# Performance work log

Measured on AMD Instinct MI355X. Metric: run time of the kernel, lower is better.

## Reference

```python
import jax, jax.numpy as jnp
import numpy as np

EPS = 1e-20
BETA = 0.25


def setup_inputs() -> dict:
    key = jax.random.key(0)
    k1, k2, k3 = jax.random.split(key, 3)
    B, N, D = 8192, 8192, 512
    x = jax.random.normal(k1, (B, D), dtype=jnp.float32)
    codebook = jax.random.normal(k2, (N, D), dtype=jnp.float32)
    u = jax.random.uniform(k3, (B, N), dtype=jnp.float32)
    return {"x": x, "codebook": codebook, "u": u}


def reference(x, codebook, u):
    # gumbel noise from uniform samples (matches sample_gumble)
    g = -jnp.log(-jnp.log(u + EPS) + EPS)  # [B, N]
    dist = (jnp.sum(x * x, axis=1, keepdims=True)
            - 2.0 * (x @ codebook.T)
            + jnp.sum(codebook * codebook, axis=1)[None, :])
    # topk(k=1) over -dist == argmin over dist
    ind = jnp.argmin(dist, axis=1)  # [B]
    # gumbel_softmax with temperature=1.0 on logits=-dist
    weights = jax.nn.softmax(-dist + g, axis=-1)  # [B, N]
    quantized = weights @ codebook  # [B, D]
    sg = jax.lax.stop_gradient
    loss = (BETA * jnp.sum((x - sg(quantized)) ** 2, axis=-1)
            + jnp.sum((sg(x) - quantized) ** 2, axis=-1))  # [B]
    return quantized, ind, loss
```

## Files before the change

kernel.cpp:

```cpp
#include <hip/hip_runtime.h>
#include <math.h>

constexpr int B = 8192, N = 8192, D = 512;
constexpr float EPSF = 1e-20f;
constexpr float SKIP   = 20.0f;
constexpr float DELTAF = 1.0f;
constexpr float DELTA  = 0.05f;
constexpr int CAP  = 96;
constexpr int DCAP = 48;

typedef short bf16x8 __attribute__((ext_vector_type(8)));
typedef float f32x4 __attribute__((ext_vector_type(4)));

__device__ inline unsigned short f2bf(float f) {
    unsigned x = __float_as_uint(f);
    unsigned r = x + 0x7FFFu + ((x >> 16) & 1u);
    return (unsigned short)(r >> 16);
}
__device__ inline float bf2f(unsigned short h) {
    return __uint_as_float(((unsigned)h) << 16);
}
__device__ inline unsigned fmap(float f) {
    unsigned b = __float_as_uint(f);
    return b ^ ((unsigned)((int)b >> 31) | 0x80000000u);
}
__device__ inline float funmap(unsigned u) {
    unsigned b = u ^ ((~(unsigned)((int)u >> 31)) | 0x80000000u);
    return __uint_as_float(b);
}
__device__ inline void gload16(const void* g, void* l) {
    __builtin_amdgcn_global_load_lds(
        (const __attribute__((address_space(1))) void*)g,
        (__attribute__((address_space(3))) void*)l, 16, 0, 0);
}


__global__ __launch_bounds__(256) void vq_prep(const float* __restrict__ x,
        const float* __restrict__ cb, unsigned short* __restrict__ ch,
        float* __restrict__ cnorm, float* __restrict__ xnorm,
        int* __restrict__ counts, int* __restrict__ dcounts) {
    int w = threadIdx.x >> 6, lane = threadIdx.x & 63;
    int gid = blockIdx.x * 256 + threadIdx.x;
    if (gid < 2 * B) { counts[gid] = 0; dcounts[gid] = 0; }
    int v = blockIdx.x * 4 + w;
    if (v < N) {
        const float4* s4 = reinterpret_cast<const float4*>(cb + (size_t)v * D) + lane * 2;
        float4 a = s4[0], c = s4[1];
        float vals[8] = {a.x, a.y, a.z, a.w, c.x, c.y, c.z, c.w};
        float ns = 0.f;
        unsigned short hb[8];
        #pragma unroll
        for (int e = 0; e < 8; ++e) {
            float vv = vals[e];
            ns += vv * vv;
            hb[e] = f2bf(vv);
        }
        #pragma unroll
        for (int off = 1; off < 64; off <<= 1) ns += __shfl_xor(ns, off);
        if (lane == 0) cnorm[v] = ns;
        *reinterpret_cast<bf16x8*>(ch + (size_t)v * D + lane * 8) = *reinterpret_cast<bf16x8*>(hb);
    } else {
        int b = v - N;
        const float4* s4 = reinterpret_cast<const float4*>(x + (size_t)b * D) + lane * 2;
        float4 a = s4[0], c = s4[1];
        float ns = a.x*a.x + a.y*a.y + a.z*a.z + a.w*a.w
                 + c.x*c.x + c.y*c.y + c.z*c.z + c.w*c.w;
        #pragma unroll
        for (int off = 1; off < 64; off <<= 1) ns += __shfl_xor(ns, off);
        if (lane == 0) xnorm[b] = ns;
    }
}

constexpr int OFF_B0 = 0;
constexpr int OFF_B1 = 65536;
constexpr int OFF_RM = 131072;
constexpr int OFF_R1 = 131328;
constexpr int OFF_CT = 131584;
constexpr int OFF_DC = 131840;
constexpr int OFF_P1 = 132096;
constexpr int OFF_P2 = 132608;
constexpr int OFF_PI = 133120;
constexpr int SMEM_BYTES = 133632;

__global__ __launch_bounds__(512, 1) void vq_mfma(
        const float* __restrict__ x, const unsigned short* __restrict__ ch,
        const float* __restrict__ cnorm, const float* __restrict__ xnorm,
        const float* __restrict__ u,
        int2* __restrict__ lists, int* __restrict__ counts,
        int* __restrict__ dlists, int* __restrict__ dcounts,
        float* __restrict__ m1h, float* __restrict__ m2h, int* __restrict__ i1h) {

    __shared__ __align__(16) unsigned char smem[SMEM_BYTES];

    const int tid = threadIdx.x, w = tid >> 6, lane = tid & 63;
    const int wm = w >> 1, wn = w & 1, l15 = lane & 15, g = lane >> 4;
    const int rg = blockIdx.x >> 1, half = blockIdx.x & 1;
    const int rbase = rg * 64, nb0 = half * 4096;

    bf16x8 ah[16];
    {
        const float* xp = x + (size_t)(rbase + wm * 16 + l15) * D + g * 8;
        #pragma unroll
        for (int ks = 0; ks < 16; ++ks) {
            const float4* p = reinterpret_cast<const float4*>(xp + ks * 32);
            float4 v0 = p[0], v1 = p[1];
            float vv[8] = {v0.x, v0.y, v0.z, v0.w, v1.x, v1.y, v1.z, v1.w};
            unsigned short hh[8];
            #pragma unroll
            for (int e = 0; e < 8; ++e) hh[e] = f2bf(vv[e]);
            ah[ks] = *reinterpret_cast<bf16x8*>(hh);
        }
    }
    float xn_r[4];
    #pragma unroll
    for (int r = 0; r < 4; ++r) xn_r[r] = xnorm[rbase + wm * 16 + g * 4 + r];

    if (tid < 64) {
        *(unsigned*)(smem + OFF_RM + tid * 4) = fmap(-INFINITY);
        *(unsigned*)(smem + OFF_R1 + tid * 4) = fmap(INFINITY);
        *(int*)(smem + OFF_CT + tid * 4) = 0;
        *(int*)(smem + OFF_DC + tid * 4) = 0;
    }

    float d1[4], d2[4], lmax[4]; int i1[4];
    #pragma unroll
    for (int r = 0; r < 4; ++r) {
        d1[r] = INFINITY; d2[r] = INFINITY; lmax[r] = -INFINITY; i1[r] = 0;
    }

    auto stage = [&](unsigned char* bbase, int nbn) {
        #pragma unroll
        for (int j = 0; j < 8; ++j) {
            const int row = w * 8 + j;
            const int c = (lane ^ j) * 8;
            gload16(ch + (size_t)(nbn + row) * D + c, bbase + row * 1024);
        }
    };

    stage(smem + OFF_B0, nb0);
    __syncthreads();

    const int colA = wn * 32 + l15;
    const int xr = colA & 7;

    #pragma unroll 1
    for (int t = 0; t < 64; ++t) {
        const int nb = nb0 + t * 64;
        if (t < 63) stage(smem + ((t & 1) ? OFF_B0 : OFF_B1), nb + 64);

        float ur[2][4];
        #pragma unroll
        for (int f = 0; f < 2; ++f)
            #pragma unroll
            for (int r = 0; r < 4; ++r)
                ur[f][r] = u[(size_t)(rbase + wm * 16 + g * 4 + r) * N + nb + wn * 32 + f * 16 + l15];
        float cn0 = cnorm[nb + wn * 32 + l15];
        float cn1 = cnorm[nb + wn * 32 + 16 + l15];

        const unsigned char* baseH = smem + ((t & 1) ? OFF_B1 : OFF_B0) + colA * 1024;
        f32x4 a0e = {0.f,0.f,0.f,0.f}, a0o = {0.f,0.f,0.f,0.f};
        f32x4 a1e = {0.f,0.f,0.f,0.f}, a1o = {0.f,0.f,0.f,0.f};
        #pragma unroll
        for (int ks = 0; ks < 16; ++ks) {
            const int pos = (((ks * 4 + g) ^ xr) << 4);
            bf16x8 b0 = *reinterpret_cast<const bf16x8*>(baseH + pos);
            bf16x8 b1 = *reinterpret_cast<const bf16x8*>(baseH + 16 * 1024 + pos);
            if (ks & 1) {
                a0o = __builtin_amdgcn_mfma_f32_16x16x32_bf16(ah[ks], b0, a0o, 0, 0, 0);
                a1o = __builtin_amdgcn_mfma_f32_16x16x32_bf16(ah[ks], b1, a1o, 0, 0, 0);
            } else {
                a0e = __builtin_amdgcn_mfma_f32_16x16x32_bf16(ah[ks], b0, a0e, 0, 0, 0);
                a1e = __builtin_amdgcn_mfma_f32_16x16x32_bf16(ah[ks], b1, a1e, 0, 0, 0);
            }
        }

        float dsv[2][4], lgv[2][4];
        #pragma unroll
        for (int f = 0; f < 2; ++f) {
            #pragma unroll
            for (int r = 0; r < 4; ++r) {
                float S = f ? (a1e[r] + a1o[r]) : (a0e[r] + a0o[r]);
                float ds = xn_r[r] - 2.f * S + (f ? cn1 : cn0);
                float gn = -__logf(-__logf(ur[f][r] + EPSF) + EPSF);
                dsv[f][r] = ds; lgv[f][r] = gn - ds;
            }
        }
        #pragma unroll
        for (int f = 0; f < 2; ++f)
            #pragma unroll
            for (int r = 0; r < 4; ++r) {
                float ds = dsv[f][r];
                int cidx = nb + wn * 32 + f * 16 + l15;
                if (ds < d1[r]) { d2[r] = d1[r]; d1[r] = ds; i1[r] = cidx; }
                else if (ds < d2[r]) d2[r] = ds;
                lmax[r] = fmaxf(lmax[r], lgv[f][r]);
            }
        if (t == 0) {
            #pragma unroll
            for (int r = 0; r < 4; ++r) {
                float mx = lmax[r], mn = d1[r];
                #pragma unroll
                for (int off = 1; off < 16; off <<= 1) {
                    mx = fmaxf(mx, __shfl_xor(mx, off));
                    mn = fminf(mn, __shfl_xor(mn, off));
                }
                if (l15 == 0) {
                    int rl = wm * 16 + g * 4 + r;
                    atomicMax((unsigned*)(smem + OFF_RM + rl * 4), fmap(mx));
                    atomicMin((unsigned*)(smem + OFF_R1 + rl * 4), fmap(mn));
                }
            }
            __syncthreads();
        }
        float rmF[4], r1F[4];
        #pragma unroll
        for (int r = 0; r < 4; ++r) {
            int rl = wm * 16 + g * 4 + r;
            rmF[r] = funmap(*(const unsigned*)(smem + OFF_RM + rl * 4));
            r1F[r] = funmap(*(const unsigned*)(smem + OFF_R1 + rl * 4));
        }
        #pragma unroll
        for (int f = 0; f < 2; ++f) {
            #pragma unroll
            for (int r = 0; r < 4; ++r) {
                const int rl = wm * 16 + g * 4 + r;
                const int grow = rbase + rl;
                float ds = dsv[f][r], lg = lgv[f][r];
                int cidx = nb + wn * 32 + f * 16 + l15;
                if (ds < fminf(r1F[r], d1[r]) + DELTAF) {
                    int slot = atomicAdd((int*)(smem + OFF_DC + rl * 4), 1);
                    if (slot < DCAP) dlists[(size_t)(half * B + grow) * DCAP + slot] = cidx;
                }
                if (ds < r1F[r]) atomicMin((unsigned*)(smem + OFF_R1 + rl * 4), fmap(ds));
                if (lg > fmaxf(rmF[r], lmax[r]) - SKIP) {
                    int slot = atomicAdd((int*)(smem + OFF_CT + rl * 4), 1);
                    if (slot < CAP)
                        lists[(size_t)(half * B + grow) * CAP + slot] =
                            make_int2(__float_as_int(lg), cidx);
                }
                if (lg > rmF[r]) atomicMax((unsigned*)(smem + OFF_RM + rl * 4), fmap(lg));
            }
        }
        __syncthreads();
    }

    #pragma unroll
    for (int r = 0; r < 4; ++r) {
        float D1 = d1[r], D2v = d2[r]; int I1 = i1[r];
        #pragma unroll
        for (int off = 1; off < 16; off <<= 1) {
            float o1 = __shfl_xor(D1, off), o2 = __shfl_xor(D2v, off);
            int oi = __shfl_xor(I1, off);
            if (o1 < D1 || (o1 == D1 && oi < I1)) { D2v = fminf(D1, o2); D1 = o1; I1 = oi; }
            else D2v = fminf(o1, D2v);
        }
        if (l15 == 0) {
            int rl = wm * 16 + g * 4 + r;
            *(float*)(smem + OFF_P1 + (wn * 64 + rl) * 4) = D1;
            *(float*)(smem + OFF_P2 + (wn * 64 + rl) * 4) = D2v;
            *(int*)(smem + OFF_PI + (wn * 64 + rl) * 4) = I1;
        }
    }
    __syncthreads();
    if (tid < 64) {
        float a1 = *(float*)(smem + OFF_P1 + tid * 4), a2 = *(float*)(smem + OFF_P2 + tid * 4);
        int ai = *(int*)(smem + OFF_PI + tid * 4);
        float b1 = *(float*)(smem + OFF_P1 + (64 + tid) * 4), b2 = *(float*)(smem + OFF_P2 + (64 + tid) * 4);
        int bi = *(int*)(smem + OFF_PI + (64 + tid) * 4);
        float m1, m2; int mi;
        if (b1 < a1 || (b1 == a1 && bi < ai)) { m1 = b1; mi = bi; m2 = fminf(a1, b2); }
        else                                  { m1 = a1; mi = ai; m2 = fminf(b1, a2); }
        int hrow = half * B + rbase + tid;
        m1h[hrow] = m1; m2h[hrow] = m2; i1h[hrow] = mi;
        counts[hrow] = *(int*)(smem + OFF_CT + tid * 4);
        dcounts[hrow] = *(int*)(smem + OFF_DC + tid * 4);
    }
}

__global__ __launch_bounds__(256) void vq_finalize(
        const float* __restrict__ cb, const float* __restrict__ x,
        const int2* __restrict__ lists, const int* __restrict__ counts,
        float* __restrict__ m1h, float* __restrict__ m2h, int* __restrict__ i1h,
        float* __restrict__ out_q, float* __restrict__ out_loss) {
    __shared__ int2 ebuf[4][2 * CAP];
    int w = threadIdx.x >> 6, lane = threadIdx.x & 63;
    int row = blockIdx.x * 4 + w;
    int n0 = counts[row];      if (n0 > CAP) n0 = CAP;
    int n1 = counts[B + row];  if (n1 > CAP) n1 = CAP;
    int n = n0 + n1;
    for (int e = lane; e < n0; e += 64) ebuf[w][e] = lists[(size_t)row * CAP + e];
    for (int e = lane; e < n1; e += 64) ebuf[w][n0 + e] = lists[(size_t)(B + row) * CAP + e];
    __syncthreads();
    float m = -INFINITY;
    for (int e = lane; e < n; e += 64) m = fmaxf(m, __int_as_float(ebuf[w][e].x));
    #pragma unroll
    for (int off = 1; off < 64; off <<= 1) m = fmaxf(m, __shfl_xor(m, off));
    float denom = 0.f;
    for (int e = lane; e < n; e += 64) denom += __expf(__int_as_float(ebuf[w][e].x) - m);
    #pragma unroll
    for (int off = 1; off < 64; off <<= 1) denom += __shfl_xor(denom, off);
    float q[8] = {0.f, 0.f, 0.f, 0.f, 0.f, 0.f, 0.f, 0.f};
    for (int e = 0; e < n; ++e) {
        int2 ent = ebuf[w][e];
        float wgt = __expf(__int_as_float(ent.x) - m);
        if (wgt < 1e-9f) continue;
        const float4* c4 = reinterpret_cast<const float4*>(cb + (size_t)ent.y * D + lane * 8);
        float4 c0 = c4[0], c1 = c4[1];
        q[0] += wgt * c0.x; q[1] += wgt * c0.y; q[2] += wgt * c0.z; q[3] += wgt * c0.w;
        q[4] += wgt * c1.x; q[5] += wgt * c1.y; q[6] += wgt * c1.z; q[7] += wgt * c1.w;
    }
    float inv = 1.f / denom;
    const float4* x4 = reinterpret_cast<const float4*>(x + (size_t)row * D + lane * 8);
    float4 xa = x4[0], xb = x4[1];
    float xs[8] = {xa.x, xa.y, xa.z, xa.w, xb.x, xb.y, xb.z, xb.w};
    float ls = 0.f;
    #pragma unroll
    for (int k = 0; k < 8; ++k) {
        q[k] *= inv;
        float dlt = xs[k] - q[k];
        ls += dlt * dlt;
    }
    float4 q0 = {q[0], q[1], q[2], q[3]}, q1 = {q[4], q[5], q[6], q[7]};
    float4* o = reinterpret_cast<float4*>(out_q + (size_t)row * D + lane * 8);
    o[0] = q0; o[1] = q1;
    #pragma unroll
    for (int off = 1; off < 64; off <<= 1) ls += __shfl_xor(ls, off);
    if (lane == 0) {
        out_loss[row] = 1.25f * ls;
        float a1 = m1h[row], a2 = m2h[row]; int ai = i1h[row];
        float b1 = m1h[B + row], b2 = m2h[B + row]; int bi = i1h[B + row];
        float mm1, mm2; int mi;
        if (b1 < a1 || (b1 == a1 && bi < ai)) { mm1 = b1; mi = bi; mm2 = fminf(a1, b2); }
        else                                  { mm1 = a1; mi = ai; mm2 = fminf(b1, a2); }
        m1h[row] = mm1; m2h[row] = mm2; i1h[row] = mi;
    }
}

__global__ __launch_bounds__(256) void vq_row_full(
        const float* __restrict__ x, const float* __restrict__ cb,
        const float* __restrict__ cnorm, const float* __restrict__ u,
        const int* __restrict__ counts,
        float* __restrict__ out_q, float* __restrict__ out_loss) {
    int row = blockIdx.x;
    if (counts[row] <= CAP && counts[B + row] <= CAP) return;
    int tid = threadIdx.x, wv_ = tid >> 6, lane = tid & 63;
    __shared__ float xs[D];
    __shared__ float red[4];
    __shared__ float wts[256]; __shared__ int ids[256]; __shared__ int nc;
    for (int i = tid; i < D; i += 256) xs[i] = x[(size_t)row * D + i];
    if (tid == 0) nc = 0;
    __syncthreads();
    float xn = 0.f;
    for (int i = tid; i < D; i += 256) xn += xs[i] * xs[i];
    #pragma unroll
    for (int off = 1; off < 64; off <<= 1) xn += __shfl_xor(xn, off);
    if (lane == 0) red[wv_] = xn;
    __syncthreads();
    xn = red[0] + red[1] + red[2] + red[3];
    __syncthreads();
    float m = -INFINITY;
    for (int n = tid; n < N; n += 256) {
        float dot = 0.f;
        const float* c = cb + (size_t)n * D;
        for (int d = 0; d < D; ++d) dot = fmaf(xs[d], c[d], dot);
        float lg = -__logf(-__logf(u[(size_t)row * N + n] + EPSF) + EPSF)
                 - (xn - 2.f * dot + cnorm[n]);
        m = fmaxf(m, lg);
    }
    #pragma unroll
    for (int off = 1; off < 64; off <<= 1) m = fmaxf(m, __shfl_xor(m, off));
    if (lane == 0) red[wv_] = m;
    __syncthreads();
    m = fmaxf(fmaxf(red[0], red[1]), fmaxf(red[2], red[3]));
    __syncthreads();
    float denom = 0.f;
    for (int n = tid; n < N; n += 256) {
        float dot = 0.f;
        const float* c = cb + (size_t)n * D;
        for (int d = 0; d < D; ++d) dot = fmaf(xs[d], c[d], dot);
        float lg = -__logf(-__logf(u[(size_t)row * N + n] + EPSF) + EPSF)
                 - (xn - 2.f * dot + cnorm[n]);
        float wv2 = __expf(lg - m);
        denom += wv2;
        if (wv2 > 1e-8f) {
            int s = atomicAdd(&nc, 1);
            if (s < 256) { wts[s] = wv2; ids[s] = n; }
        }
    }
    #pragma unroll
    for (int off = 1; off < 64; off <<= 1) denom += __shfl_xor(denom, off);
    if (lane == 0) red[wv_] = denom;
    __syncthreads();
    denom = red[0] + red[1] + red[2] + red[3];
    int ncl = nc < 256 ? nc : 256;
    float q0 = 0.f, q1 = 0.f;
    for (int e = 0; e < ncl; ++e) {
        const float* c = cb + (size_t)ids[e] * D;
        q0 += wts[e] * c[tid * 2];
        q1 += wts[e] * c[tid * 2 + 1];
    }
    q0 /= denom; q1 /= denom;
    out_q[(size_t)row * D + tid * 2] = q0;
    out_q[(size_t)row * D + tid * 2 + 1] = q1;
    float dl0 = xs[tid * 2] - q0, dl1 = xs[tid * 2 + 1] - q1;
    float ls = dl0 * dl0 + dl1 * dl1;
    #pragma unroll
    for (int off = 1; off < 64; off <<= 1) ls += __shfl_xor(ls, off);
    __syncthreads();
    if (lane == 0) red[wv_] = ls;
    __syncthreads();
    if (tid == 0) out_loss[row] = 1.25f * (red[0] + red[1] + red[2] + red[3]);
}

__global__ __launch_bounds__(256) void argmin_fix2(
        const float* __restrict__ x, const float* __restrict__ cb,
        const float* __restrict__ m1h, const float* __restrict__ m2h,
        const int* __restrict__ i1h,
        const int* __restrict__ dcounts, const int* __restrict__ dlists,
        float* __restrict__ out_ind) {
    int w = threadIdx.x >> 6, lane = threadIdx.x & 63;
    int row = blockIdx.x * 4 + w;
    if (m2h[row] - m1h[row] >= DELTAF) {
        if (lane == 0) out_ind[row] = (float)i1h[row];
        return;
    }
    const float4* x4 = reinterpret_cast<const float4*>(x + (size_t)row * D) + lane * 2;
    float4 xa = x4[0], xb = x4[1];
    double xd[8] = {(double)xa.x, (double)xa.y, (double)xa.z, (double)xa.w,
                    (double)xb.x, (double)xb.y, (double)xb.z, (double)xb.w};
    double bestv = 1e300; int besti = 0x7fffffff;

    auto evalCode = [&](int n) {
        const float4* c4 = reinterpret_cast<const float4*>(cb + (size_t)n * D) + lane * 2;
        float4 ca = c4[0], cbv = c4[1];
        double cd[8] = {(double)ca.x, (double)ca.y, (double)ca.z, (double)ca.w,
                        (double)cbv.x, (double)cbv.y, (double)cbv.z, (double)cbv.w};
        double s = 0.0;
        #pragma unroll
        for (int k = 0; k < 8; ++k) {
            double dlt = xd[k] - cd[k];
            s = fma(dlt, dlt, s);
        }
        #pragma unroll
        for (int off = 1; off < 64; off <<= 1) s += __shfl_xor(s, off);
        if (s < bestv || (s == bestv && n < besti)) { bestv = s; besti = n; }
    };

    int n0 = dcounts[row], n1 = dcounts[B + row];
    if (n0 <= DCAP && n1 <= DCAP) {
        evalCode(i1h[row]);
        for (int e = 0; e < n0; ++e) evalCode(dlists[(size_t)row * DCAP + e]);
        for (int e = 0; e < n1; ++e) evalCode(dlists[(size_t)(B + row) * DCAP + e]);
    } else {
        for (int n = 0; n < N; ++n) evalCode(n);
    }
    if (lane == 0) out_ind[row] = (float)besti;
}

constexpr int ROWS = 16;
constexpr int NT   = 256;
constexpr int DT   = 16;

__global__ __launch_bounds__(256) void prep_norms(const float* __restrict__ x,
                                                  const float* __restrict__ cb,
                                                  float* __restrict__ cnorm,
                                                  float* __restrict__ xnorm) {
    int wave = threadIdx.x >> 6, lane = threadIdx.x & 63;
    int v = blockIdx.x * 4 + wave;
    const float* src;
    float* dst;
    if (v < N) { src = cb + (size_t)v * D; dst = cnorm + v; }
    else       { int b = v - N; if (b >= B) return; src = x + (size_t)b * D; dst = xnorm + b; }
    const float4* s4 = reinterpret_cast<const float4*>(src) + lane * 2;
    float4 a = s4[0], c = s4[1];
    float s = a.x*a.x + a.y*a.y + a.z*a.z + a.w*a.w
            + c.x*c.x + c.y*c.y + c.z*c.z + c.w*c.w;
    #pragma unroll
    for (int off = 1; off < 64; off <<= 1) s += __shfl_xor(s, off);
    if (lane == 0) *dst = s;
}

__global__ __launch_bounds__(256) void vq_main(const float* __restrict__ x,
        const float* __restrict__ cb, const float* __restrict__ u,
        const float* __restrict__ cnorm, const float* __restrict__ xnorm,
        float* __restrict__ out_q, float* __restrict__ out_loss,
        float* __restrict__ m1w, float* __restrict__ m2w, int* __restrict__ i1w) {

    __shared__ float xs[ROWS][D];
    __shared__ float ct[DT][NT];

    const int tid  = threadIdx.x;
    const int wave = tid >> 6, lane = tid & 63;
    const int rbase = blockIdx.x * ROWS;
    const int wrow  = rbase + wave * 4;

    for (int i = tid; i < ROWS * (D / 4); i += 256)
        reinterpret_cast<float4*>(xs)[i] =
            reinterpret_cast<const float4*>(x + (size_t)rbase * D)[i];
    __syncthreads();

    float xn[4];
    #pragma unroll
    for (int r = 0; r < 4; ++r) xn[r] = xnorm[wrow + r];

    float m[4], denom[4], acc[4][8];
    float am1[4], am2[4]; int ai1[4];
    #pragma unroll
    for (int r = 0; r < 4; ++r) {
        m[r] = -INFINITY; denom[r] = 0.f;
        am1[r] = INFINITY; am2[r] = INFINITY; ai1[r] = 0;
        #pragma unroll
        for (int k = 0; k < 8; ++k) acc[r][k] = 0.f;
    }

    for (int nb = 0; nb < N; nb += NT) {
        float S[4][4];
        #pragma unroll
        for (int r = 0; r < 4; ++r)
            #pragma unroll
            for (int j = 0; j < 4; ++j) S[r][j] = 0.f;

        for (int db = 0; db < D; db += DT) {
            __syncthreads();
            {
                const float4* src = reinterpret_cast<const float4*>(
                        cb + (size_t)(nb + tid) * D + db);
                float4 a0 = src[0], a1 = src[1], a2 = src[2], a3 = src[3];
                ct[ 0][tid]=a0.x; ct[ 1][tid]=a0.y; ct[ 2][tid]=a0.z; ct[ 3][tid]=a0.w;
                ct[ 4][tid]=a1.x; ct[ 5][tid]=a1.y; ct[ 6][tid]=a1.z; ct[ 7][tid]=a1.w;
                ct[ 8][tid]=a2.x; ct[ 9][tid]=a2.y; ct[10][tid]=a2.z; ct[11][tid]=a2.w;
                ct[12][tid]=a3.x; ct[13][tid]=a3.y; ct[14][tid]=a3.z; ct[15][tid]=a3.w;
            }
            __syncthreads();
            #pragma unroll
            for (int dq = 0; dq < DT / 4; ++dq) {
                float creg[4][4];
                #pragma unroll
                for (int k = 0; k < 4; ++k) {
                    float4 cv = *reinterpret_cast<const float4*>(&ct[dq*4 + k][4*lane]);
                    creg[k][0]=cv.x; creg[k][1]=cv.y; creg[k][2]=cv.z; creg[k][3]=cv.w;
                }
                #pragma unroll
                for (int r = 0; r < 4; ++r) {
                    float4 xv = *reinterpret_cast<const float4*>(&xs[wave*4 + r][db + dq*4]);
                    float xr[4] = {xv.x, xv.y, xv.z, xv.w};
                    #pragma unroll
                    for (int k = 0; k < 4; ++k)
                        #pragma unroll
                        for (int j = 0; j < 4; ++j)
                            S[r][j] = fmaf(xr[k], creg[k][j], S[r][j]);
                }
            }
        }

        float4 cn4 = *reinterpret_cast<const float4*>(&cnorm[nb + 4*lane]);
        float cn[4] = {cn4.x, cn4.y, cn4.z, cn4.w};

        float logit[4][4], dist[4][4];
        #pragma unroll
        for (int r = 0; r < 4; ++r) {
            float4 u4 = *reinterpret_cast<const float4*>(
                    &u[(size_t)(wrow + r) * N + nb + 4*lane]);
            float uu[4] = {u4.x, u4.y, u4.z, u4.w};
            #pragma unroll
            for (int j = 0; j < 4; ++j) {
                float ds = xn[r] - 2.f * S[r][j] + cn[j];
                float gg  = -logf(-logf(uu[j] + EPSF) + EPSF);
                dist[r][j]  = ds;
                logit[r][j] = gg - ds;
            }
        }

        #pragma unroll
        for (int r = 0; r < 4; ++r) {
            float l1 = INFINITY, l2 = INFINITY; int li = 0;
            #pragma unroll
            for (int j = 0; j < 4; ++j) {
                float dv = dist[r][j]; int idx = nb + 4*lane + j;
                if (dv < l1)      { l2 = l1; l1 = dv; li = idx; }
                else if (dv < l2) { l2 = dv; }
            }
            #pragma unroll
            for (int off = 1; off < 64; off <<= 1) {
                float o1 = __shfl_xor(l1, off), o2 = __shfl_xor(l2, off);
                int   oi = __shfl_xor(li, off);
                if (o1 < l1 || (o1 == l1 && oi < li)) { l2 = fminf(l1, o2); l1 = o1; li = oi; }
                else                                  { l2 = fminf(o1, l2); }
            }
            if (l1 < am1[r] || (l1 == am1[r] && li < ai1[r])) {
                am2[r] = fminf(am1[r], l2); am1[r] = l1; ai1[r] = li;
            } else {
                am2[r] = fminf(am2[r], l1);
            }

            float lm = fmaxf(fmaxf(logit[r][0], logit[r][1]),
                             fmaxf(logit[r][2], logit[r][3]));
            #pragma unroll
            for (int off = 1; off < 64; off <<= 1) lm = fmaxf(lm, __shfl_xor(lm, off));
            if (lm > m[r]) {
                float s = expf(m[r] - lm);
                denom[r] *= s;
                #pragma unroll
                for (int k = 0; k < 8; ++k) acc[r][k] *= s;
                m[r] = lm;
            }

            float wv[4];
            #pragma unroll
            for (int j = 0; j < 4; ++j) {
                float e = logit[r][j] - m[r];
                bool act = e > -SKIP;
                wv[j] = act ? expf(e) : 0.f;
                denom[r] += wv[j];
            }
            #pragma unroll
            for (int j = 0; j < 4; ++j) {
                unsigned long long mk = __ballot(wv[j] > 0.f);
                while (mk) {
                    int L = __ffsll((unsigned long long)mk) - 1;
                    mk &= mk - 1;
                    float wb = __shfl(wv[j], L);
                    int nstar = nb + 4*L + j;
                    const float4* crow = reinterpret_cast<const float4*>(
                            cb + (size_t)nstar * D + 8*lane);
                    float4 c0 = crow[0], c1 = crow[1];
                    acc[r][0] = fmaf(wb, c0.x, acc[r][0]);
                    acc[r][1] = fmaf(wb, c0.y, acc[r][1]);
                    acc[r][2] = fmaf(wb, c0.z, acc[r][2]);
                    acc[r][3] = fmaf(wb, c0.w, acc[r][3]);
                    acc[r][4] = fmaf(wb, c1.x, acc[r][4]);
                    acc[r][5] = fmaf(wb, c1.y, acc[r][5]);
                    acc[r][6] = fmaf(wb, c1.z, acc[r][6]);
                    acc[r][7] = fmaf(wb, c1.w, acc[r][7]);
                }
            }
        }
    }

    #pragma unroll
    for (int r = 0; r < 4; ++r) {
        float dn = denom[r];
        #pragma unroll
        for (int off = 1; off < 64; off <<= 1) dn += __shfl_xor(dn, off);
        float inv = 1.f / dn;
        int row = wrow + r;
        float q[8]; float ls = 0.f;
        #pragma unroll
        for (int k = 0; k < 8; ++k) {
            q[k] = acc[r][k] * inv;
            float dlt = xs[wave*4 + r][8*lane + k] - q[k];
            ls += dlt * dlt;
        }
        float4 q0 = {q[0], q[1], q[2], q[3]}, q1 = {q[4], q[5], q[6], q[7]};
        float4* o = reinterpret_cast<float4*>(out_q + (size_t)row * D + 8*lane);
        o[0] = q0; o[1] = q1;
        #pragma unroll
        for (int off = 1; off < 64; off <<= 1) ls += __shfl_xor(ls, off);
        if (lane == 0) {
            out_loss[row] = 1.25f * ls;
            m1w[row] = am1[r]; m2w[row] = am2[r]; i1w[row] = ai1[r];
        }
    }
}

__global__ __launch_bounds__(256) void argmin_fix(const float* __restrict__ x,
        const float* __restrict__ cb, const float* __restrict__ m1w,
        const float* __restrict__ m2w, const int* __restrict__ i1w,
        float* __restrict__ out_ind) {
    int b = blockIdx.x, tid = threadIdx.x;
    if (m2w[b] - m1w[b] >= DELTA) {
        if (tid == 0) out_ind[b] = (float)i1w[b];
        return;
    }
    __shared__ double xsd[D];
    for (int i = tid; i < D; i += 256) xsd[i] = (double)x[(size_t)b * D + i];
    __syncthreads();
    double xn = 0.0;
    for (int d = 0; d < D; ++d) xn += xsd[d] * xsd[d];

    double bestv = 1e300; int besti = N;
    for (int n = tid; n < N; n += 256) {
        const float* c = cb + (size_t)n * D;
        double d0 = 0.0, d1v = 0.0, c0 = 0.0, c1v = 0.0;
        for (int d = 0; d < D; d += 2) {
            double ca = (double)c[d], cbv = (double)c[d + 1];
            d0 += xsd[d] * ca;  c0 += ca * ca;
            d1v += xsd[d + 1] * cbv; c1v += cbv * cbv;
        }
        double dv = xn - 2.0 * (d0 + d1v) + (c0 + c1v);
        if (dv < bestv || (dv == bestv && n < besti)) { bestv = dv; besti = n; }
    }
    __shared__ double rv[256]; __shared__ int ri[256];
    rv[tid] = bestv; ri[tid] = besti;
    __syncthreads();
    for (int s = 128; s > 0; s >>= 1) {
        if (tid < s) {
            if (rv[tid+s] < rv[tid] || (rv[tid+s] == rv[tid] && ri[tid+s] < ri[tid])) {
                rv[tid] = rv[tid+s]; ri[tid] = ri[tid+s];
            }
        }
        __syncthreads();
    }
    if (tid == 0) out_ind[b] = (float)ri[0];
}

extern "C" void kernel_launch(void* const* d_in, const int* in_sizes, int n_in,
                              void* d_out, int out_size, void* d_ws, size_t ws_size,
                              hipStream_t stream) {
    const float* x  = (const float*)d_in[0];
    const float* cb = (const float*)d_in[1];
    const float* u  = (const float*)d_in[2];
    float* out      = (float*)d_out;
    float* out_q    = out;
    float* out_ind  = out + (size_t)B * D;
    float* out_loss = out_ind + B;

    const size_t O_CH = 0;
    const size_t O_CN = O_CH + (size_t)N * D * 2;
    const size_t O_XN = O_CN + (size_t)N * 4;
    const size_t O_M1 = O_XN + (size_t)B * 4;
    const size_t O_M2 = O_M1 + (size_t)2 * B * 4;
    const size_t O_I1 = O_M2 + (size_t)2 * B * 4;
    const size_t O_CT = O_I1 + (size_t)2 * B * 4;
    const size_t O_DC = O_CT + (size_t)2 * B * 4;
    const size_t O_LS = O_DC + (size_t)2 * B * 4;
    const size_t O_DL = O_LS + (size_t)2 * B * CAP * 8;
    const size_t NEED = O_DL + (size_t)2 * B * DCAP * 4;

    if (ws_size >= NEED) {
        char* w8 = (char*)d_ws;
        unsigned short* ch = (unsigned short*)(w8 + O_CH);
        float* cnorm = (float*)(w8 + O_CN);
        float* xnorm = (float*)(w8 + O_XN);
        float* m1h   = (float*)(w8 + O_M1);
        float* m2h   = (float*)(w8 + O_M2);
        int*   i1h   = (int*)(w8 + O_I1);
        int*   counts= (int*)(w8 + O_CT);
        int*   dcounts=(int*)(w8 + O_DC);
        int2*  lists = (int2*)(w8 + O_LS);
        int*   dlists= (int*)(w8 + O_DL);

        hipLaunchKernelGGL(vq_prep, dim3((N + B) / 4), dim3(256), 0, stream,
                           x, cb, ch, cnorm, xnorm, counts, dcounts);
        hipLaunchKernelGGL(vq_mfma, dim3(256), dim3(512), 0, stream,
                           x, ch, cnorm, xnorm, u, lists, counts,
                           dlists, dcounts, m1h, m2h, i1h);
        hipLaunchKernelGGL(vq_finalize, dim3(B / 4), dim3(256), 0, stream,
                           cb, x, lists, counts, m1h, m2h, i1h, out_q, out_loss);
        hipLaunchKernelGGL(vq_row_full, dim3(B), dim3(256), 0, stream,
                           x, cb, cnorm, u, counts, out_q, out_loss);
        hipLaunchKernelGGL(argmin_fix2, dim3(B / 4), dim3(256), 0, stream,
                           x, cb, m1h, m2h, i1h, dcounts, dlists, out_ind);
    } else {
        float* ws    = (float*)d_ws;
        float* cnorm = ws;
        float* xnorm = ws + N;
        float* m1w   = xnorm + B;
        float* m2w   = m1w + B;
        int*   i1w   = (int*)(m2w + B);

        hipLaunchKernelGGL(prep_norms, dim3((N + B) / 4), dim3(256), 0, stream,
                           x, cb, cnorm, xnorm);
        hipLaunchKernelGGL(vq_main, dim3(B / ROWS), dim3(256), 0, stream,
                           x, cb, u, cnorm, xnorm, out_q, out_loss, m1w, m2w, i1w);
        hipLaunchKernelGGL(argmin_fix, dim3(B), dim3(256), 0, stream,
                           x, cb, m1w, m2w, i1w, out_ind);
    }
}
```

Baseline: 302.9 us.

## Prefetch uniform noise one tile ahead and skip Gumbel logs for hopeless candidates

```diff
diff --git a/kernel.cpp b/kernel.cpp
--- a/kernel.cpp
+++ b/kernel.cpp
@@ -4,6 +4,7 @@
 constexpr int B = 8192, N = 8192, D = 512;
 constexpr float EPSF = 1e-20f;
 constexpr float SKIP   = 20.0f;
+constexpr float GMAX   = 17.0f;
 constexpr float DELTAF = 1.0f;
 constexpr float DELTA  = 0.05f;
 constexpr int CAP  = 96;
@@ -138,6 +139,15 @@
     };
 
     stage(smem + OFF_B0, nb0);
+
+    const float* ubase = u + (size_t)(rbase + wm * 16 + g * 4) * N + wn * 32 + l15;
+    float ur[2][4];
+    #pragma unroll
+    for (int f = 0; f < 2; ++f)
+        #pragma unroll
+        for (int r = 0; r < 4; ++r)
+            ur[f][r] = ubase[(size_t)r * N + f * 16 + nb0];
+
     __syncthreads();
 
     const int colA = wn * 32 + l15;
@@ -148,12 +158,14 @@
         const int nb = nb0 + t * 64;
         if (t < 63) stage(smem + ((t & 1) ? OFF_B0 : OFF_B1), nb + 64);
 
-        float ur[2][4];
-        #pragma unroll
-        for (int f = 0; f < 2; ++f)
-            #pragma unroll
-            for (int r = 0; r < 4; ++r)
-                ur[f][r] = u[(size_t)(rbase + wm * 16 + g * 4 + r) * N + nb + wn * 32 + f * 16 + l15];
+        float urN[2][4];
+        if (t < 63) {
+            #pragma unroll
+            for (int f = 0; f < 2; ++f)
+                #pragma unroll
+                for (int r = 0; r < 4; ++r)
+                    urN[f][r] = ubase[(size_t)r * N + f * 16 + nb + 64];
+        }
         float cn0 = cnorm[nb + wn * 32 + l15];
         float cn1 = cnorm[nb + wn * 32 + 16 + l15];
 
@@ -174,28 +186,29 @@
             }
         }
 
-        float dsv[2][4], lgv[2][4];
-        #pragma unroll
-        for (int f = 0; f < 2; ++f) {
+        float dsv[2][4];
+        #pragma unroll
+        for (int f = 0; f < 2; ++f)
             #pragma unroll
             for (int r = 0; r < 4; ++r) {
                 float S = f ? (a1e[r] + a1o[r]) : (a0e[r] + a0o[r]);
-                float ds = xn_r[r] - 2.f * S + (f ? cn1 : cn0);
-                float gn = -__logf(-__logf(ur[f][r] + EPSF) + EPSF);
-                dsv[f][r] = ds; lgv[f][r] = gn - ds;
-            }
-        }
-        #pragma unroll
-        for (int f = 0; f < 2; ++f)
-            #pragma unroll
-            for (int r = 0; r < 4; ++r) {
-                float ds = dsv[f][r];
-                int cidx = nb + wn * 32 + f * 16 + l15;
-                if (ds < d1[r]) { d2[r] = d1[r]; d1[r] = ds; i1[r] = cidx; }
-                else if (ds < d2[r]) d2[r] = ds;
-                lmax[r] = fmaxf(lmax[r], lgv[f][r]);
-            }
+                dsv[f][r] = xn_r[r] - 2.f * S + (f ? cn1 : cn0);
+            }
+
         if (t == 0) {
+            float lgv0[2][4];
+            #pragma unroll
+            for (int f = 0; f < 2; ++f)
+                #pragma unroll
+                for (int r = 0; r < 4; ++r) {
+                    float ds = dsv[f][r];
+                    float gn = -__logf(-__logf(ur[f][r] + EPSF) + EPSF);
+                    lgv0[f][r] = gn - ds;
+                    int cidx = nb + wn * 32 + f * 16 + l15;
+                    if (ds < d1[r]) { d2[r] = d1[r]; d1[r] = ds; i1[r] = cidx; }
+                    else if (ds < d2[r]) d2[r] = ds;
+                    lmax[r] = fmaxf(lmax[r], lgv0[f][r]);
+                }
             #pragma unroll
             for (int r = 0; r < 4; ++r) {
                 float mx = lmax[r], mn = d1[r];
@@ -211,35 +224,78 @@
                 }
             }
             __syncthreads();
-        }
-        float rmF[4], r1F[4];
-        #pragma unroll
-        for (int r = 0; r < 4; ++r) {
-            int rl = wm * 16 + g * 4 + r;
-            rmF[r] = funmap(*(const unsigned*)(smem + OFF_RM + rl * 4));
-            r1F[r] = funmap(*(const unsigned*)(smem + OFF_R1 + rl * 4));
-        }
-        #pragma unroll
-        for (int f = 0; f < 2; ++f) {
+            float rmF[4], r1F[4];
             #pragma unroll
             for (int r = 0; r < 4; ++r) {
-                const int rl = wm * 16 + g * 4 + r;
-                const int grow = rbase + rl;
-                float ds = dsv[f][r], lg = lgv[f][r];
-                int cidx = nb + wn * 32 + f * 16 + l15;
-                if (ds < fminf(r1F[r], d1[r]) + DELTAF) {
-                    int slot = atomicAdd((int*)(smem + OFF_DC + rl * 4), 1);
-                    if (slot < DCAP) dlists[(size_t)(half * B + grow) * DCAP + slot] = cidx;
+                int rl = wm * 16 + g * 4 + r;
+                rmF[r] = funmap(*(const unsigned*)(smem + OFF_RM + rl * 4));
+                r1F[r] = funmap(*(const unsigned*)(smem + OFF_R1 + rl * 4));
+            }
+            #pragma unroll
+            for (int f = 0; f < 2; ++f)
+                #pragma unroll
+                for (int r = 0; r < 4; ++r) {
+                    const int rl = wm * 16 + g * 4 + r;
+                    const int grow = rbase + rl;
+                    float ds = dsv[f][r], lg = lgv0[f][r];
+                    int cidx = nb + wn * 32 + f * 16 + l15;
+                    if (ds < fminf(r1F[r], d1[r]) + DELTAF) {
+                        int slot = atomicAdd((int*)(smem + OFF_DC + rl * 4), 1);
+                        if (slot < DCAP) dlists[(size_t)(half * B + grow) * DCAP + slot] = cidx;
+                    }
+                    if (ds < r1F[r]) atomicMin((unsigned*)(smem + OFF_R1 + rl * 4), fmap(ds));
+                    if (lg > fmaxf(rmF[r], lmax[r]) - SKIP) {
+                        int slot = atomicAdd((int*)(smem + OFF_CT + rl * 4), 1);
+                        if (slot < CAP)
+                            lists[(size_t)(half * B + grow) * CAP + slot] =
+                                make_int2(__float_as_int(lg), cidx);
+                    }
+                    if (lg > rmF[r]) atomicMax((unsigned*)(smem + OFF_RM + rl * 4), fmap(lg));
                 }
-                if (ds < r1F[r]) atomicMin((unsigned*)(smem + OFF_R1 + rl * 4), fmap(ds));
-                if (lg > fmaxf(rmF[r], lmax[r]) - SKIP) {
-                    int slot = atomicAdd((int*)(smem + OFF_CT + rl * 4), 1);
-                    if (slot < CAP)
-                        lists[(size_t)(half * B + grow) * CAP + slot] =
-                            make_int2(__float_as_int(lg), cidx);
+        } else {
+            float rmF[4], r1F[4];
+            #pragma unroll
+            for (int r = 0; r < 4; ++r) {
+                int rl = wm * 16 + g * 4 + r;
+                rmF[r] = funmap(*(const unsigned*)(smem + OFF_RM + rl * 4));
+                r1F[r] = funmap(*(const unsigned*)(smem + OFF_R1 + rl * 4));
+            }
+            #pragma unroll
+            for (int f = 0; f < 2; ++f)
+                #pragma unroll
+                for (int r = 0; r < 4; ++r) {
+                    const int rl = wm * 16 + g * 4 + r;
+                    const int grow = rbase + rl;
+                    float ds = dsv[f][r];
+                    int cidx = nb + wn * 32 + f * 16 + l15;
+                    if (ds < d1[r]) { d2[r] = d1[r]; d1[r] = ds; i1[r] = cidx; }
+                    else if (ds < d2[r]) d2[r] = ds;
+                    bool need = (ds < fminf(r1F[r], d1[r]) + DELTAF)
+                             || (ds < GMAX + SKIP - fmaxf(rmF[r], lmax[r]));
+                    if (__any(need)) {
+                        float gn = -__logf(-__logf(ur[f][r] + EPSF) + EPSF);
+                        float lg = gn - ds;
+                        lmax[r] = fmaxf(lmax[r], lg);
+                        if (ds < fminf(r1F[r], d1[r]) + DELTAF) {
+                            int slot = atomicAdd((int*)(smem + OFF_DC + rl * 4), 1);
+                            if (slot < DCAP) dlists[(size_t)(half * B + grow) * DCAP + slot] = cidx;
+                        }
+                        if (ds < r1F[r]) atomicMin((unsigned*)(smem + OFF_R1 + rl * 4), fmap(ds));
+                        if (lg > fmaxf(rmF[r], lmax[r]) - SKIP) {
+                            int slot = atomicAdd((int*)(smem + OFF_CT + rl * 4), 1);
+                            if (slot < CAP)
+                                lists[(size_t)(half * B + grow) * CAP + slot] =
+                                    make_int2(__float_as_int(lg), cidx);
+                        }
+                        if (lg > rmF[r]) atomicMax((unsigned*)(smem + OFF_RM + rl * 4), fmap(lg));
+                    }
                 }
-                if (lg > rmF[r]) atomicMax((unsigned*)(smem + OFF_RM + rl * 4), fmap(lg));
-            }
+        }
+        if (t < 63) {
+            #pragma unroll
+            for (int f = 0; f < 2; ++f)
+                #pragma unroll
+                for (int r = 0; r < 4; ++r) ur[f][r] = urN[f][r];
         }
         __syncthreads();
     }
```

Measured after the change: 300.3 us. No clear change (-0.9%).
